# Performance work log

Measured on AMD Instinct MI355X. Metric: run time of the kernel, lower is better.

## Reference

```python
import jax, jax.numpy as jnp
from jax import lax
import numpy as np

SHIFT_LAT = 20.0
SHIFT_LON = 20.0
ROT_RANGE = 10.0
BASE_MPP = 0.8
MPPS = [BASE_MPP * 2 ** (3 - l) for l in range(4)]  # [6.4, 3.2, 1.6, 0.8]
AS = [16, 32, 64, 128]
CS = [64, 32, 16, 8]
B = 8


def setup_inputs() -> dict:
    key = jax.random.key(0)
    ks = jax.random.split(key, 15)
    inp = {}
    for l in range(4):
        inp[f"grd_feat{l}"] = jax.random.normal(ks[l], (B, CS[l], AS[l], AS[l]), jnp.float32)
        inp[f"sat_feat{l}"] = jax.random.normal(ks[4 + l], (B, CS[l], AS[l], AS[l]), jnp.float32)
        inp[f"grd_mask{l}"] = jax.random.uniform(ks[8 + l], (1, AS[l], AS[l]), jnp.float32)
    inp["gt_shift_u"] = jax.random.uniform(ks[12], (B, 1), jnp.float32)
    inp["gt_shift_v"] = jax.random.uniform(ks[13], (B, 1), jnp.float32)
    inp["gt_heading"] = jax.random.uniform(ks[14], (B, 1), jnp.float32)
    return inp


def _level_corr(sat, grd, mask, mpp):
    # sat, grd: (B, C, A, A); mask: (1, A, A)
    Bb, C, A, _ = sat.shape
    g = grd * mask[:, None, :, :]  # broadcast over B, C (== repeat(B,C,1,1))
    crop_H = int(A - SHIFT_LAT * 3 / mpp)
    crop_W = int(A - SHIFT_LON * 3 / mpp)
    top = int(round((A - crop_H) / 2.0))   # torchvision center_crop
    left = int(round((A - crop_W) / 2.0))
    g2s = g[:, :, top:top + crop_H, left:left + crop_W]
    flat = g2s.reshape(Bb, -1)
    norm = jnp.linalg.norm(flat, axis=1, keepdims=True)  # F.normalize, eps=1e-12
    g2s = (flat / jnp.maximum(norm, 1e-12)).reshape(Bb, C, crop_H, crop_W)
    # per-sample cross-correlation via grouped conv: lhs (1, B*C, A, A), rhs (B, C, cH, cW)
    s = sat.reshape(1, Bb * C, A, A)
    corr = lax.conv_general_dilated(
        s, g2s, window_strides=(1, 1), padding='VALID',
        feature_group_count=Bb,
        dimension_numbers=('NCHW', 'OIHW', 'NCHW'))[0]  # (B, corr_H, corr_W)
    # L2-norm grouped conv with full-extent mask kernel -> per-sample scalar
    sq = jnp.einsum('bchw,hw->b', sat * sat, mask[0])
    denom = jnp.maximum(jnp.sqrt(sq + 1e-8), 1e-6)[:, None, None]  # (B,1,1)
    return 2.0 - 2.0 * corr / denom


def _forward(grd_feats, sat_feats, masks, gt_shift_u, gt_shift_v, gt_heading):
    corr_maps = [_level_corr(sat_feats[l], grd_feats[l], masks[l], MPPS[l])
                 for l in range(4)]
    cos = jnp.cos(gt_heading[:, 0] * ROT_RANGE / 180.0 * jnp.pi)
    sin = jnp.sin(gt_heading[:, 0] * ROT_RANGE / 180.0 * jnp.pi)
    gt_dx = -gt_shift_u[:, 0] * SHIFT_LON
    gt_dy = -gt_shift_v[:, 0] * SHIFT_LAT
    dx_rot = -gt_dx * cos + gt_dy * sin
    dy_rot = gt_dx * sin + gt_dy * cos
    losses = []
    for l in range(4):
        corr = corr_maps[l]
        Bb, cH, cW = corr.shape
        w = jnp.round(cW / 2 - 0.5 + dx_rot / MPPS[l]).astype(jnp.int32)
        h = jnp.round(cH / 2 - 0.5 + dy_rot / MPPS[l]).astype(jnp.int32)
        pos = corr[jnp.arange(Bb), h, w]          # (B,)
        pos_neg = pos[:, None, None] - corr       # (B, cH, cW)
        loss = jnp.sum(jnp.logaddexp(0.0, pos_neg * 10.0)) / (Bb * (cH * cW - 1))
        losses.append(loss)
    return jnp.sum(jnp.stack(losses))


def reference(grd_feat0, grd_feat1, grd_feat2, grd_feat3,
              sat_feat0, sat_feat1, sat_feat2, sat_feat3,
              grd_mask0, grd_mask1, grd_mask2, grd_mask3,
              gt_shift_u, gt_shift_v, gt_heading):
    return _forward(
        [grd_feat0, grd_feat1, grd_feat2, grd_feat3],
        [sat_feat0, sat_feat1, sat_feat2, sat_feat3],
        [grd_mask0, grd_mask1, grd_mask2, grd_mask3],
        gt_shift_u, gt_shift_v, gt_heading)
```

## Files before the change

### kernel.cpp

```cpp
#include <hip/hip_runtime.h>
#include <math.h>


#define WS_SC 0
#define WS_PART 32
#define WS_CORR 1056
#define N_ENTRIES 62544
#define PB0 63600
#define PB1 65536
#define PB2 78336
#define PB3 175680
#define WS_NEED_BYTES 3700000

__device__ __forceinline__ float block_sum256(float v, float* sw) {
#pragma unroll
  for (int o = 32; o > 0; o >>= 1) v += __shfl_down(v, o, 64);
  if ((threadIdx.x & 63) == 0) sw[threadIdx.x >> 6] = v;
  __syncthreads();
  float r = (threadIdx.x < 4) ? sw[threadIdx.x] : 0.0f;
  r += __shfl_down(r, 2, 64);
  r += __shfl_down(r, 1, 64);
  __syncthreads();
  return r;
}

__global__ __launch_bounds__(256) void init_kernel(float* __restrict__ ws,
                                                   float* __restrict__ out) {
  const int e = blockIdx.x * 256 + threadIdx.x;
  if (e < N_ENTRIES) ws[WS_CORR + e] = 0.0f;
  if (e == 0) out[0] = 0.0f;
}

template <int C, int A, int CROP, int TOP>
__device__ void prep_partial_level(const float* __restrict__ grd,
                                   const float* __restrict__ sat,
                                   const float* __restrict__ mask, int b, int k,
                                   float* __restrict__ part, float* sw) {
  const float* gb = grd + (size_t)b * C * A * A;
  float s1 = 0.0f;
  constexpr int N1 = C * CROP * CROP;
  for (int idx = k * 256 + (int)threadIdx.x; idx < N1; idx += 4096) {
    int c = idx / (CROP * CROP);
    int r = idx - c * (CROP * CROP);
    int h = r / CROP;
    int w = r - h * CROP;
    float m = mask[(TOP + h) * A + (TOP + w)];
    float g = gb[((size_t)c * A + (TOP + h)) * A + (TOP + w)] * m;
    s1 += g * g;
  }
  s1 = block_sum256(s1, sw);
  const float4* sb = (const float4*)(sat + (size_t)b * C * A * A);
  const float4* m4 = (const float4*)mask;
  float s2 = 0.0f;
  constexpr int NV = C * A * A / 4;
  constexpr int MV = A * A / 4;
  for (int v = k * 256 + (int)threadIdx.x; v < NV; v += 4096) {
    float4 sv = sb[v];
    float4 mv = m4[v & (MV - 1)];
    s2 += sv.x * sv.x * mv.x + sv.y * sv.y * mv.y + sv.z * sv.z * mv.z +
          sv.w * sv.w * mv.w;
  }
  s2 = block_sum256(s2, sw);
  if (threadIdx.x == 0) {
    part[0] = s1;
    part[1] = s2;
  }
}

__global__ __launch_bounds__(256) void prep_partial_kernel(
    const float* g0, const float* s0, const float* m0, const float* g1,
    const float* s1, const float* m1, const float* g2, const float* s2,
    const float* m2, const float* g3, const float* s3, const float* m3,
    float* ws) {
  __shared__ float sw[4];
  const int pair = blockIdx.x >> 4;
  const int k = blockIdx.x & 15;
  const int lev = pair >> 3;
  const int b = pair & 7;
  float* part = ws + WS_PART + (pair * 16 + k) * 2;
  if (lev == 0)      prep_partial_level<64, 16, 6, 5>(g0, s0, m0, b, k, part, sw);
  else if (lev == 1) prep_partial_level<32, 32, 13, 10>(g1, s1, m1, b, k, part, sw);
  else if (lev == 2) prep_partial_level<16, 64, 26, 19>(g2, s2, m2, b, k, part, sw);
  else               prep_partial_level<8, 128, 53, 38>(g3, s3, m3, b, k, part, sw);
}

__global__ __launch_bounds__(64) void prep_final_kernel(float* __restrict__ ws) {
  const int t = threadIdx.x;
  if (t < 32) {
    float s1 = 0.0f, s2 = 0.0f;
    const float* p = ws + WS_PART + t * 32;
    for (int k = 0; k < 16; ++k) {
      s1 += p[2 * k];
      s2 += p[2 * k + 1];
    }
    float norm = sqrtf(s1);
    float denom = fmaxf(sqrtf(s2 + 1e-8f), 1e-6f);
    ws[WS_SC + t] = 2.0f / (fmaxf(norm, 1e-12f) * denom);
  }
}

template <bool PARTIAL, int PBASE, int C, int A, int CROP, int TOP, int OH,
          int TJ8, int NTILES, int CSPLIT, int RSPLIT, int CHUNKS, int START>
__device__ void corr_level(int rel, int wv, int lane,
                           const float* __restrict__ grd,
                           const float* __restrict__ sat,
                           const float* __restrict__ mask,
                           float* __restrict__ ws, float* g_lds,
                           float* r_lds) {
  constexpr int CSP = C / CSPLIT;
  constexpr int OW = OH;
  constexpr int RS4 = (CROP + 3) & ~3;
  constexpr int NV8 = (CROP + 7 + 3) / 4;
  constexpr int TAIL = CROP + 7 - 4 * (NV8 - 1);
  constexpr int NPACK = CSPLIT * RSPLIT / 4;
  constexpr int E = 8 * OH * OW;
  const int b = rel / (CHUNKS * NPACK);
  int r2 = rel - b * (CHUNKS * NPACK);
  const int chunk = r2 / NPACK;
  const int pack = r2 - chunk * NPACK;
  const int sl = pack * 4 + wv;
  const int cs = sl / RSPLIT;
  const int rs = sl - cs * RSPLIT;
  const int c0 = cs * CSP;
  const int r0 = (rs * CROP) / RSPLIT;
  const int r1 = ((rs + 1) * CROP) / RSPLIT;
  const int nr = r1 - r0;

  const float* gb = grd + (size_t)(b * C + c0) * A * A;
  for (int c = 0; c < CSP; ++c)
    for (int h = 0; h < nr; ++h)
      if (lane < RS4)
        g_lds[(c * nr + h) * RS4 + lane] =
            (lane < CROP)
                ? gb[((size_t)c * A + (TOP + r0 + h)) * A + (TOP + lane)] *
                      mask[(TOP + r0 + h) * A + (TOP + lane)]
                : 0.0f;
  __syncthreads();

  const int s = chunk * 64 + lane;
  const bool active = s < NTILES;
  const int ss = active ? s : 0;
  const int ii = ss / TJ8;
  const int jj = ss - ii * TJ8;
  const int i0 = min(ii * 4, OH - 4);
  const int j0 = min(jj * 8, OW - 8);
  const int own_i = ii * 4 - i0;
  const int own_j = jj * 8 - j0;
  const int amax = A - 1 - j0;

  float acc[4][8] = {};
  const float* sb =
      sat + (size_t)(b * C + c0) * A * A + (size_t)(i0 + r0) * A + j0;
#pragma unroll 1
  for (int c = 0; c < CSP; ++c) {
    const float* satc = sb + (size_t)c * A * A;
    const float* gl = g_lds + c * nr * RS4;
#pragma unroll 1
    for (int r = 0; r < nr + 3; ++r) {
      float rbuf[NV8 * 4];
      const float* srow = satc + (size_t)r * A;
#pragma unroll
      for (int k = 0; k < NV8 - 1; ++k) {
        float4 t = *(const float4*)(srow + 4 * k);
        rbuf[4 * k + 0] = t.x;
        rbuf[4 * k + 1] = t.y;
        rbuf[4 * k + 2] = t.z;
        rbuf[4 * k + 3] = t.w;
      }
#pragma unroll
      for (int q = 0; q < TAIL; ++q) {
        const int idx = 4 * (NV8 - 1) + q;
        rbuf[idx] = (idx <= amax) ? srow[idx] : 0.0f;
      }
#pragma unroll
      for (int ti = 0; ti < 4; ++ti) {
        const int h = r - ti;
        if ((unsigned)h < (unsigned)nr) {
          const float* grow = gl + h * RS4;
#pragma unroll
          for (int w4 = 0; w4 < RS4 / 4; ++w4) {
            const float4 gq = *(const float4*)(grow + 4 * w4);
#pragma unroll
            for (int gi = 0; gi < 4; ++gi) {
              const int w = 4 * w4 + gi;
              if (w < CROP) {
                const float g = (gi == 0) ? gq.x : (gi == 1) ? gq.y
                                : (gi == 2) ? gq.z : gq.w;
#pragma unroll
                for (int tj = 0; tj < 8; ++tj)
                  acc[ti][tj] = fmaf(rbuf[w + tj], g, acc[ti][tj]);
              }
            }
          }
        }
      }
    }
  }

#pragma unroll
  for (int p = 0; p < 2; ++p) {
    if (p) __syncthreads();
#pragma unroll
    for (int k2 = 0; k2 < 16; ++k2) {
      const int gk = p * 16 + k2;
      r_lds[(k2 * 4 + wv) * 64 + lane] = acc[gk >> 3][gk & 7];
    }
    __syncthreads();
#pragma unroll
    for (int kk = 0; kk < 4; ++kk) {
      const int k2 = wv * 4 + kk;
      const int gk = p * 16 + k2;
      const int ti = gk >> 3;
      const int tj = gk & 7;
      const float v = r_lds[(k2 * 4 + 0) * 64 + lane] +
                      r_lds[(k2 * 4 + 1) * 64 + lane] +
                      r_lds[(k2 * 4 + 2) * 64 + lane] +
                      r_lds[(k2 * 4 + 3) * 64 + lane];
      if (active && ti >= own_i && tj >= own_j) {
        const int addr = ((b * OH + i0 + ti) * OW) + j0 + tj;
        if constexpr (PARTIAL)
          ws[PBASE + pack * E + addr] = v;
        else
          atomicAdd(ws + WS_CORR + START + addr, v);
      }
    }
  }
}

template <bool PARTIAL>
__global__ __launch_bounds__(256, 1) void corr_kernel(
    const float* g0, const float* s0, const float* m0, const float* g1,
    const float* s1, const float* m1, const float* g2, const float* s2,
    const float* m2, const float* g3, const float* s3, const float* m3,
    float* ws) {
  __shared__ float g_lds[4 * 416];
  __shared__ float r_lds[16 * 4 * 64];
  const int wv = threadIdx.x >> 6;
  const int lane = threadIdx.x & 63;
  float* gl = g_lds + wv * 416;
  const int bid = blockIdx.x;
  if (bid < 16)
    corr_level<PARTIAL, PB0, 64, 16, 6, 5, 11, 2, 6, 8, 1, 1, 0>(
        bid, wv, lane, g0, s0, m0, ws, gl, r_lds);
  else if (bid < 48)
    corr_level<PARTIAL, PB1, 32, 32, 13, 10, 20, 3, 15, 16, 1, 1, 968>(
        bid - 16, wv, lane, g1, s1, m1, ws, gl, r_lds);
  else if (bid < 112)
    corr_level<PARTIAL, PB2, 16, 64, 26, 19, 39, 5, 50, 8, 4, 1, 4168>(
        bid - 48, wv, lane, g2, s2, m2, ws, gl, r_lds);
  else
    corr_level<PARTIAL, PB3, 8, 128, 53, 38, 76, 10, 190, 8, 8, 3, 16336>(
        bid - 112, wv, lane, g3, s3, m3, ws, gl, r_lds);
}

__global__ __launch_bounds__(256) void reduce_kernel(float* __restrict__ ws) {
  const int e = blockIdx.x * 256 + threadIdx.x;
  if (e >= N_ENTRIES) return;
  int np, base, E, r;
  if (e < 968)        { np = 2;  base = PB0; E = 968;   r = e; }
  else if (e < 4168)  { np = 4;  base = PB1; E = 3200;  r = e - 968; }
  else if (e < 16336) { np = 8;  base = PB2; E = 12168; r = e - 4168; }
  else                { np = 16; base = PB3; E = 46208; r = e - 16336; }
  float s = 0.0f;
  for (int p = 0; p < np; ++p) s += ws[base + p * E + r];
  ws[WS_CORR + e] = s;
}

__global__ __launch_bounds__(256) void loss_kernel(const float* __restrict__ u,
                                                   const float* __restrict__ v,
                                                   const float* __restrict__ hd,
                                                   const float* __restrict__ ws,
                                                   float* __restrict__ out) {
  __shared__ float sw[4];
  const int e = blockIdx.x * 256 + threadIdx.x;
  float term = 0.0f;
  if (e < N_ENTRIES) {
    int lev, start, OH;
    float mpp;
    if (e < 968)        { lev = 0; start = 0;     OH = 11; mpp = 6.4f; }
    else if (e < 4168)  { lev = 1; start = 968;   OH = 20; mpp = 3.2f; }
    else if (e < 16336) { lev = 2; start = 4168;  OH = 39; mpp = 1.6f; }
    else                { lev = 3; start = 16336; OH = 76; mpp = 0.8f; }
    const int r = e - start;
    const int ow2 = OH * OH;
    const int b = r / ow2;
    const float scv = ws[WS_SC + lev * 8 + b];
    float t = hd[b] * 10.0f;
    t = t / 180.0f;
    t = t * 3.14159265358979323846f;
    const float cs = cosf(t), sn = sinf(t);
    const float gdx = -u[b] * 20.0f;
    const float gdy = -v[b] * 20.0f;
    const float dxr = -gdx * cs + gdy * sn;
    const float dyr = gdx * sn + gdy * cs;
    int wi = (int)rintf(OH * 0.5f - 0.5f + dxr / mpp);
    int hi = (int)rintf(OH * 0.5f - 0.5f + dyr / mpp);
    wi = min(max(wi, 0), OH - 1);
    hi = min(max(hi, 0), OH - 1);
    const float raw = ws[WS_CORR + e];
    const float rp = ws[WS_CORR + start + (b * OH + hi) * OH + wi];
    const float z = 10.0f * scv * (raw - rp);
    const float spl = fmaxf(z, 0.0f) + log1pf(expf(-fabsf(z)));
    term = spl / (8.0f * (float)(ow2 - 1));
  }
  const float tot = block_sum256(term, sw);
  if (threadIdx.x == 0) atomicAdd(out, tot);
}

extern "C" void kernel_launch(void* const* d_in, const int* in_sizes, int n_in,
                              void* d_out, int out_size, void* d_ws,
                              size_t ws_size, hipStream_t stream) {
  const float* g0 = (const float*)d_in[0];
  const float* s0 = (const float*)d_in[1];
  const float* m0 = (const float*)d_in[2];
  const float* g1 = (const float*)d_in[3];
  const float* s1 = (const float*)d_in[4];
  const float* m1 = (const float*)d_in[5];
  const float* g2 = (const float*)d_in[6];
  const float* s2 = (const float*)d_in[7];
  const float* m2 = (const float*)d_in[8];
  const float* g3 = (const float*)d_in[9];
  const float* s3 = (const float*)d_in[10];
  const float* m3 = (const float*)d_in[11];
  const float* u  = (const float*)d_in[12];
  const float* v  = (const float*)d_in[13];
  const float* hd = (const float*)d_in[14];
  float* ws = (float*)d_ws;
  float* out = (float*)d_out;
  const bool use_partial = (ws_size >= (size_t)WS_NEED_BYTES);

  init_kernel<<<dim3(245), dim3(256), 0, stream>>>(ws, out);
  prep_partial_kernel<<<dim3(512), dim3(256), 0, stream>>>(
      g0, s0, m0, g1, s1, m1, g2, s2, m2, g3, s3, m3, ws);
  prep_final_kernel<<<dim3(1), dim3(64), 0, stream>>>(ws);
  if (use_partial) {
    corr_kernel<true><<<dim3(496), dim3(256), 0, stream>>>(
        g0, s0, m0, g1, s1, m1, g2, s2, m2, g3, s3, m3, ws);
    reduce_kernel<<<dim3(245), dim3(256), 0, stream>>>(ws);
  } else {
    corr_kernel<false><<<dim3(496), dim3(256), 0, stream>>>(
        g0, s0, m0, g1, s1, m1, g2, s2, m2, g3, s3, m3, ws);
  }
  loss_kernel<<<dim3(245), dim3(256), 0, stream>>>(u, v, hd, ws, out);
}
```

Baseline: 75.39 us.

## Pad ground tiles in LDS and drop row-validity branches in correlation inner loop

Each wave's ground crop slice in LDS gets three zero rows above and below. The inner loop can then read the four kernel rows for all four output rows with no per-row bounds test, software-prefetches the next float4 of each row, and issues the four row FMAs per satellite value together. Block dispatch order is reversed so the heavy level-3 blocks start first, for better load balance. This costs more shared memory per block and some wasted FMAs on the zero padding rows.

```diff
diff --git a/kernel.cpp b/kernel.cpp
--- a/kernel.cpp
+++ b/kernel.cpp
@@ -125,16 +125,19 @@
   const int r0 = (rs * CROP) / RSPLIT;
   const int r1 = ((rs + 1) * CROP) / RSPLIT;
   const int nr = r1 - r0;
+  const int nrp = nr + 6;
 
   const float* gb = grd + (size_t)(b * C + c0) * A * A;
   for (int c = 0; c < CSP; ++c)
-    for (int h = 0; h < nr; ++h)
-      if (lane < RS4)
-        g_lds[(c * nr + h) * RS4 + lane] =
-            (lane < CROP)
-                ? gb[((size_t)c * A + (TOP + r0 + h)) * A + (TOP + lane)] *
-                      mask[(TOP + r0 + h) * A + (TOP + lane)]
-                : 0.0f;
+    for (int hh = 0; hh < nrp; ++hh)
+      if (lane < RS4) {
+        const int h = hh - 3;
+        float v = 0.0f;
+        if (h >= 0 && h < nr && lane < CROP)
+          v = gb[((size_t)c * A + (TOP + r0 + h)) * A + (TOP + lane)] *
+              mask[(TOP + r0 + h) * A + (TOP + lane)];
+        g_lds[(c * nrp + hh) * RS4 + lane] = v;
+      }
   __syncthreads();
 
   const int s = chunk * 64 + lane;
@@ -154,7 +157,7 @@
 #pragma unroll 1
   for (int c = 0; c < CSP; ++c) {
     const float* satc = sb + (size_t)c * A * A;
-    const float* gl = g_lds + c * nr * RS4;
+    const float* glc = g_lds + c * nrp * RS4;
 #pragma unroll 1
     for (int r = 0; r < nr + 3; ++r) {
       float rbuf[NV8 * 4];
@@ -172,27 +175,48 @@
         const int idx = 4 * (NV8 - 1) + q;
         rbuf[idx] = (idx <= amax) ? srow[idx] : 0.0f;
       }
-#pragma unroll
-      for (int ti = 0; ti < 4; ++ti) {
-        const int h = r - ti;
-        if ((unsigned)h < (unsigned)nr) {
-          const float* grow = gl + h * RS4;
-#pragma unroll
-          for (int w4 = 0; w4 < RS4 / 4; ++w4) {
-            const float4 gq = *(const float4*)(grow + 4 * w4);
-#pragma unroll
-            for (int gi = 0; gi < 4; ++gi) {
-              const int w = 4 * w4 + gi;
-              if (w < CROP) {
-                const float g = (gi == 0) ? gq.x : (gi == 1) ? gq.y
-                                : (gi == 2) ? gq.z : gq.w;
-#pragma unroll
-                for (int tj = 0; tj < 8; ++tj)
-                  acc[ti][tj] = fmaf(rbuf[w + tj], g, acc[ti][tj]);
-              }
+      const float* p3 = glc + (size_t)r * RS4;
+      const float* p2 = p3 + RS4;
+      const float* p1 = p3 + 2 * RS4;
+      const float* p0 = p3 + 3 * RS4;
+      float4 q0 = *(const float4*)p0;
+      float4 q1 = *(const float4*)p1;
+      float4 q2 = *(const float4*)p2;
+      float4 q3 = *(const float4*)p3;
+#pragma unroll
+      for (int w4 = 0; w4 < RS4 / 4; ++w4) {
+        float4 n0, n1, n2, n3;
+        if (w4 + 1 < RS4 / 4) {
+          n0 = *(const float4*)(p0 + 4 * (w4 + 1));
+          n1 = *(const float4*)(p1 + 4 * (w4 + 1));
+          n2 = *(const float4*)(p2 + 4 * (w4 + 1));
+          n3 = *(const float4*)(p3 + 4 * (w4 + 1));
+        } else {
+          n0 = q0; n1 = q1; n2 = q2; n3 = q3;
+        }
+#pragma unroll
+        for (int gi = 0; gi < 4; ++gi) {
+          const int w = 4 * w4 + gi;
+          if (w < CROP) {
+            const float f0 = (gi == 0) ? q0.x : (gi == 1) ? q0.y
+                             : (gi == 2) ? q0.z : q0.w;
+            const float f1 = (gi == 0) ? q1.x : (gi == 1) ? q1.y
+                             : (gi == 2) ? q1.z : q1.w;
+            const float f2 = (gi == 0) ? q2.x : (gi == 1) ? q2.y
+                             : (gi == 2) ? q2.z : q2.w;
+            const float f3 = (gi == 0) ? q3.x : (gi == 1) ? q3.y
+                             : (gi == 2) ? q3.z : q3.w;
+#pragma unroll
+            for (int tj = 0; tj < 8; ++tj) {
+              const float sv = rbuf[w + tj];
+              acc[0][tj] = fmaf(sv, f0, acc[0][tj]);
+              acc[1][tj] = fmaf(sv, f1, acc[1][tj]);
+              acc[2][tj] = fmaf(sv, f2, acc[2][tj]);
+              acc[3][tj] = fmaf(sv, f3, acc[3][tj]);
             }
           }
         }
+        q0 = n0; q1 = n1; q2 = n2; q3 = n3;
       }
     }
   }
@@ -233,24 +257,24 @@
     const float* s1, const float* m1, const float* g2, const float* s2,
     const float* m2, const float* g3, const float* s3, const float* m3,
     float* ws) {
-  __shared__ float g_lds[4 * 416];
+  __shared__ float g_lds[4 * 768];
   __shared__ float r_lds[16 * 4 * 64];
   const int wv = threadIdx.x >> 6;
   const int lane = threadIdx.x & 63;
-  float* gl = g_lds + wv * 416;
+  float* gl = g_lds + wv * 768;
   const int bid = blockIdx.x;
-  if (bid < 16)
+  if (bid < 384)
+    corr_level<PARTIAL, PB3, 8, 128, 53, 38, 76, 10, 190, 8, 8, 3, 16336>(
+        bid, wv, lane, g3, s3, m3, ws, gl, r_lds);
+  else if (bid < 448)
+    corr_level<PARTIAL, PB2, 16, 64, 26, 19, 39, 5, 50, 8, 4, 1, 4168>(
+        bid - 384, wv, lane, g2, s2, m2, ws, gl, r_lds);
+  else if (bid < 480)
+    corr_level<PARTIAL, PB1, 32, 32, 13, 10, 20, 3, 15, 16, 1, 1, 968>(
+        bid - 448, wv, lane, g1, s1, m1, ws, gl, r_lds);
+  else
     corr_level<PARTIAL, PB0, 64, 16, 6, 5, 11, 2, 6, 8, 1, 1, 0>(
-        bid, wv, lane, g0, s0, m0, ws, gl, r_lds);
-  else if (bid < 48)
-    corr_level<PARTIAL, PB1, 32, 32, 13, 10, 20, 3, 15, 16, 1, 1, 968>(
-        bid - 16, wv, lane, g1, s1, m1, ws, gl, r_lds);
-  else if (bid < 112)
-    corr_level<PARTIAL, PB2, 16, 64, 26, 19, 39, 5, 50, 8, 4, 1, 4168>(
-        bid - 48, wv, lane, g2, s2, m2, ws, gl, r_lds);
-  else
-    corr_level<PARTIAL, PB3, 8, 128, 53, 38, 76, 10, 190, 8, 8, 3, 16336>(
-        bid - 112, wv, lane, g3, s3, m3, ws, gl, r_lds);
+        bid - 480, wv, lane, g0, s0, m0, ws, gl, r_lds);
 }
 
 __global__ __launch_bounds__(256) void reduce_kernel(float* __restrict__ ws) {
```

Result: slower. 82.42 us (+9.3%).

## Fuse prep and correlation kernels, merge reduce into loss, drop init launch

Applied to the files above, without the earlier changes.

The partial-workspace path now launches three kernels instead of six. The norm-partial blocks run inside the correlation kernel as extra blocks, and init and prep_final are removed. The partial-sum reduction and the per-sample scale computation move into the loss kernel, which writes per-block sums that a single-block final kernel adds up deterministically. Block order is also changed so the largest level is scheduled first, which should balance the load better. In exchange, the loss kernel rereads all partial planes and recomputes each sample's scale per thread.

```diff
diff --git a/kernel.cpp b/kernel.cpp
--- a/kernel.cpp
+++ b/kernel.cpp
@@ -227,8 +227,107 @@
   }
 }
 
-template <bool PARTIAL>
-__global__ __launch_bounds__(256, 1) void corr_kernel(
+__global__ __launch_bounds__(256, 1) void fused_kernel(
+    const float* g0, const float* s0, const float* m0, const float* g1,
+    const float* s1, const float* m1, const float* g2, const float* s2,
+    const float* m2, const float* g3, const float* s3, const float* m3,
+    float* ws) {
+  __shared__ float g_lds[4 * 416];
+  __shared__ float r_lds[16 * 4 * 64];
+  __shared__ float sw[4];
+  const int bid = blockIdx.x;
+  if (bid < 496) {
+    const int wv = threadIdx.x >> 6;
+    const int lane = threadIdx.x & 63;
+    float* gl = g_lds + wv * 416;
+    if (bid < 384)
+      corr_level<true, PB3, 8, 128, 53, 38, 76, 10, 190, 8, 8, 3, 16336>(
+          bid, wv, lane, g3, s3, m3, ws, gl, r_lds);
+    else if (bid < 448)
+      corr_level<true, PB2, 16, 64, 26, 19, 39, 5, 50, 8, 4, 1, 4168>(
+          bid - 384, wv, lane, g2, s2, m2, ws, gl, r_lds);
+    else if (bid < 480)
+      corr_level<true, PB1, 32, 32, 13, 10, 20, 3, 15, 16, 1, 1, 968>(
+          bid - 448, wv, lane, g1, s1, m1, ws, gl, r_lds);
+    else
+      corr_level<true, PB0, 64, 16, 6, 5, 11, 2, 6, 8, 1, 1, 0>(
+          bid - 480, wv, lane, g0, s0, m0, ws, gl, r_lds);
+  } else {
+    const int pb = bid - 496;
+    const int pair = pb >> 4;
+    const int k = pb & 15;
+    const int lev = pair >> 3;
+    const int b = pair & 7;
+    float* part = ws + WS_PART + (pair * 16 + k) * 2;
+    if (lev == 0)      prep_partial_level<64, 16, 6, 5>(g0, s0, m0, b, k, part, sw);
+    else if (lev == 1) prep_partial_level<32, 32, 13, 10>(g1, s1, m1, b, k, part, sw);
+    else if (lev == 2) prep_partial_level<16, 64, 26, 19>(g2, s2, m2, b, k, part, sw);
+    else               prep_partial_level<8, 128, 53, 38>(g3, s3, m3, b, k, part, sw);
+  }
+}
+
+__global__ __launch_bounds__(256) void loss2_kernel(const float* __restrict__ u,
+                                                    const float* __restrict__ v,
+                                                    const float* __restrict__ hd,
+                                                    float* __restrict__ ws) {
+  __shared__ float sw[4];
+  const int e = blockIdx.x * 256 + threadIdx.x;
+  float term = 0.0f;
+  if (e < N_ENTRIES) {
+    int lev, start, OH, np, base, E;
+    float mpp;
+    if (e < 968)        { lev = 0; start = 0;     OH = 11; mpp = 6.4f; np = 2;  base = PB0; E = 968; }
+    else if (e < 4168)  { lev = 1; start = 968;   OH = 20; mpp = 3.2f; np = 4;  base = PB1; E = 3200; }
+    else if (e < 16336) { lev = 2; start = 4168;  OH = 39; mpp = 1.6f; np = 8;  base = PB2; E = 12168; }
+    else                { lev = 3; start = 16336; OH = 76; mpp = 0.8f; np = 16; base = PB3; E = 46208; }
+    const int r = e - start;
+    const int ow2 = OH * OH;
+    const int b = r / ow2;
+    const float* p = ws + WS_PART + (lev * 8 + b) * 32;
+    float s1 = 0.0f, s2 = 0.0f;
+    for (int kk = 0; kk < 16; ++kk) {
+      s1 += p[2 * kk];
+      s2 += p[2 * kk + 1];
+    }
+    const float norm = sqrtf(s1);
+    const float denom = fmaxf(sqrtf(s2 + 1e-8f), 1e-6f);
+    const float scv = 2.0f / (fmaxf(norm, 1e-12f) * denom);
+    float t = hd[b] * 10.0f;
+    t = t / 180.0f;
+    t = t * 3.14159265358979323846f;
+    const float cs = cosf(t), sn = sinf(t);
+    const float gdx = -u[b] * 20.0f;
+    const float gdy = -v[b] * 20.0f;
+    const float dxr = -gdx * cs + gdy * sn;
+    const float dyr = gdx * sn + gdy * cs;
+    int wi = (int)rintf(OH * 0.5f - 0.5f + dxr / mpp);
+    int hi = (int)rintf(OH * 0.5f - 0.5f + dyr / mpp);
+    wi = min(max(wi, 0), OH - 1);
+    hi = min(max(hi, 0), OH - 1);
+    const int posoff = (b * OH + hi) * OH + wi;
+    float raw = 0.0f, rp = 0.0f;
+    for (int pp = 0; pp < np; ++pp) {
+      raw += ws[base + pp * E + r];
+      rp += ws[base + pp * E + posoff];
+    }
+    const float z = 10.0f * scv * (raw - rp);
+    const float spl = fmaxf(z, 0.0f) + log1pf(expf(-fabsf(z)));
+    term = spl / (8.0f * (float)(ow2 - 1));
+  }
+  const float tot = block_sum256(term, sw);
+  if (threadIdx.x == 0) ws[WS_CORR + blockIdx.x] = tot;
+}
+
+__global__ __launch_bounds__(256) void final_kernel(const float* __restrict__ ws,
+                                                    float* __restrict__ out) {
+  __shared__ float sw[4];
+  const int t = threadIdx.x;
+  float v = (t < 245) ? ws[WS_CORR + t] : 0.0f;
+  const float tot = block_sum256(v, sw);
+  if (t == 0) out[0] = tot;
+}
+
+__global__ __launch_bounds__(256, 1) void corr_kernel_fb(
     const float* g0, const float* s0, const float* m0, const float* g1,
     const float* s1, const float* m1, const float* g2, const float* s2,
     const float* m2, const float* g3, const float* s3, const float* m3,
@@ -239,31 +338,18 @@
   const int lane = threadIdx.x & 63;
   float* gl = g_lds + wv * 416;
   const int bid = blockIdx.x;
-  if (bid < 16)
-    corr_level<PARTIAL, PB0, 64, 16, 6, 5, 11, 2, 6, 8, 1, 1, 0>(
-        bid, wv, lane, g0, s0, m0, ws, gl, r_lds);
-  else if (bid < 48)
-    corr_level<PARTIAL, PB1, 32, 32, 13, 10, 20, 3, 15, 16, 1, 1, 968>(
-        bid - 16, wv, lane, g1, s1, m1, ws, gl, r_lds);
-  else if (bid < 112)
-    corr_level<PARTIAL, PB2, 16, 64, 26, 19, 39, 5, 50, 8, 4, 1, 4168>(
-        bid - 48, wv, lane, g2, s2, m2, ws, gl, r_lds);
+  if (bid < 384)
+    corr_level<false, PB3, 8, 128, 53, 38, 76, 10, 190, 8, 8, 3, 16336>(
+        bid, wv, lane, g3, s3, m3, ws, gl, r_lds);
+  else if (bid < 448)
+    corr_level<false, PB2, 16, 64, 26, 19, 39, 5, 50, 8, 4, 1, 4168>(
+        bid - 384, wv, lane, g2, s2, m2, ws, gl, r_lds);
+  else if (bid < 480)
+    corr_level<false, PB1, 32, 32, 13, 10, 20, 3, 15, 16, 1, 1, 968>(
+        bid - 448, wv, lane, g1, s1, m1, ws, gl, r_lds);
   else
-    corr_level<PARTIAL, PB3, 8, 128, 53, 38, 76, 10, 190, 8, 8, 3, 16336>(
-        bid - 112, wv, lane, g3, s3, m3, ws, gl, r_lds);
-}
-
-__global__ __launch_bounds__(256) void reduce_kernel(float* __restrict__ ws) {
-  const int e = blockIdx.x * 256 + threadIdx.x;
-  if (e >= N_ENTRIES) return;
-  int np, base, E, r;
-  if (e < 968)        { np = 2;  base = PB0; E = 968;   r = e; }
-  else if (e < 4168)  { np = 4;  base = PB1; E = 3200;  r = e - 968; }
-  else if (e < 16336) { np = 8;  base = PB2; E = 12168; r = e - 4168; }
-  else                { np = 16; base = PB3; E = 46208; r = e - 16336; }
-  float s = 0.0f;
-  for (int p = 0; p < np; ++p) s += ws[base + p * E + r];
-  ws[WS_CORR + e] = s;
+    corr_level<false, PB0, 64, 16, 6, 5, 11, 2, 6, 8, 1, 1, 0>(
+        bid - 480, wv, lane, g0, s0, m0, ws, gl, r_lds);
 }
 
 __global__ __launch_bounds__(256) void loss_kernel(const float* __restrict__ u,
@@ -329,17 +415,18 @@
   float* out = (float*)d_out;
   const bool use_partial = (ws_size >= (size_t)WS_NEED_BYTES);
 
-  init_kernel<<<dim3(245), dim3(256), 0, stream>>>(ws, out);
-  prep_partial_kernel<<<dim3(512), dim3(256), 0, stream>>>(
-      g0, s0, m0, g1, s1, m1, g2, s2, m2, g3, s3, m3, ws);
-  prep_final_kernel<<<dim3(1), dim3(64), 0, stream>>>(ws);
   if (use_partial) {
-    corr_kernel<true><<<dim3(496), dim3(256), 0, stream>>>(
+    fused_kernel<<<dim3(1008), dim3(256), 0, stream>>>(
         g0, s0, m0, g1, s1, m1, g2, s2, m2, g3, s3, m3, ws);
-    reduce_kernel<<<dim3(245), dim3(256), 0, stream>>>(ws);
+    loss2_kernel<<<dim3(245), dim3(256), 0, stream>>>(u, v, hd, ws);
+    final_kernel<<<dim3(1), dim3(256), 0, stream>>>(ws, out);
   } else {
-    corr_kernel<false><<<dim3(496), dim3(256), 0, stream>>>(
+    init_kernel<<<dim3(245), dim3(256), 0, stream>>>(ws, out);
+    prep_partial_kernel<<<dim3(512), dim3(256), 0, stream>>>(
         g0, s0, m0, g1, s1, m1, g2, s2, m2, g3, s3, m3, ws);
-  }
-  loss_kernel<<<dim3(245), dim3(256), 0, stream>>>(u, v, hd, ws, out);
-}
+    prep_final_kernel<<<dim3(1), dim3(64), 0, stream>>>(ws);
+    corr_kernel_fb<<<dim3(496), dim3(256), 0, stream>>>(
+        g0, s0, m0, g1, s1, m1, g2, s2, m2, g3, s3, m3, ws);
+    loss_kernel<<<dim3(245), dim3(256), 0, stream>>>(u, v, hd, ws, out);
+  }
+}
```

After: 72.48 us. 1.04x faster.
